# Kernel tuning notes

Hardware: AMD Instinct MI355X
Metric: run time of the kernel (lower is better)

The kernel has to match this reference:

```python
import jax, jax.numpy as jnp
import numpy as np

D_MODEL = 1024
NUM_HEADS = 16
HEAD_DIM = D_MODEL // NUM_HEADS
BATCH, SEQ = 2, 2048


def setup_inputs() -> dict:
    key = jax.random.key(0)
    k1, k2, k3, k4, k5 = jax.random.split(key, 5)
    x = jax.random.normal(k1, (BATCH, SEQ, D_MODEL), dtype=jnp.float32)
    mask = jnp.ones((BATCH, SEQ), dtype=jnp.int32)
    s = 1.0 / np.sqrt(D_MODEL)
    W_qkv = jax.random.uniform(k2, (D_MODEL, 3 * D_MODEL), jnp.float32, -s, s)
    b_qkv = jax.random.uniform(k3, (3 * D_MODEL,), jnp.float32, -s, s)
    W_proj = jax.random.uniform(k4, (D_MODEL, D_MODEL), jnp.float32, -s, s)
    b_proj = jax.random.uniform(k5, (D_MODEL,), jnp.float32, -s, s)
    return {"x": x, "mask": mask, "W_qkv": W_qkv, "b_qkv": b_qkv,
            "W_proj": W_proj, "b_proj": b_proj}


def reference(x, mask, W_qkv, b_qkv, W_proj, b_proj):
    B, S, _ = x.shape
    qkv = x @ W_qkv + b_qkv                                  # [B,S,3D]
    q, k, v = jnp.split(qkv, 3, axis=-1)
    def heads(t):  # [B,S,D] -> [B,H,S,hd]
        return t.reshape(B, S, NUM_HEADS, HEAD_DIM).transpose(0, 2, 1, 3)
    q, k, v = heads(q), heads(k), heads(v)
    scores = jnp.einsum('bhqd,bhkd->bhqk', q, k) / np.sqrt(HEAD_DIM)
    # mask: [B,S] key-padding -> [B,1,1,S], positions where mask==0 get -inf
    scores = jnp.where(mask[:, None, None, :] == 0, -jnp.inf, scores)
    attn = jax.nn.softmax(scores, axis=-1)
    ctx = jnp.einsum('bhqk,bhkd->bhqd', attn, v)             # [B,H,S,hd]
    ctx = ctx.transpose(0, 2, 1, 3).reshape(B, S, D_MODEL)
    return ctx @ W_proj + b_proj
```

## Files before the change

kernel.cpp:

```cpp
#include <hip/hip_runtime.h>


#define BATCH 2
#define SEQ 2048
#define DMODEL 1024
#define NHEADS 16
#define HDIM 64
#define BS (BATCH * SEQ)
#define N3 (3 * DMODEL)
#define QSCALE 0.18033688011112042f

typedef float f32x4 __attribute__((ext_vector_type(4)));
typedef float f32x16 __attribute__((ext_vector_type(16)));
typedef short bf16x8 __attribute__((ext_vector_type(8)));
typedef unsigned short u16;
typedef unsigned short u16x4 __attribute__((ext_vector_type(4)));

typedef const __attribute__((address_space(1))) unsigned int* gptr_t;
typedef __attribute__((address_space(3))) unsigned int* sptr_t;

__device__ __forceinline__ u16 f2bf(float f) {
  unsigned int u = __float_as_uint(f);
  return (u16)((u + 0x7fffu + ((u >> 16) & 1u)) >> 16);
}

__device__ __forceinline__ void gload_lds16(const void* g, void* l) {
  __builtin_amdgcn_global_load_lds((gptr_t)g, (sptr_t)l, 16, 0, 0);
}

__device__ __forceinline__ unsigned cvtpk(float lo, float hi) {
  unsigned r;
  asm("v_cvt_pk_bf16_f32 %0, %1, %2" : "=v"(r) : "v"(lo), "v"(hi));
  return r;
}

__device__ __forceinline__ void pl32swap(unsigned& d, unsigned& s) {
  asm volatile("v_permlane32_swap_b32 %0, %1" : "+v"(d), "+v"(s));
}

#define WAIT_VM4() asm volatile("s_waitcnt vmcnt(4)" ::: "memory")
#define WAIT_VM0() asm volatile("s_waitcnt vmcnt(0)" ::: "memory")

__global__ __launch_bounds__(256) void conv_x(const float* __restrict__ in,
                                              u16* __restrict__ out, int n4) {
  int i = blockIdx.x * 256 + threadIdx.x;
  if (i >= n4) return;
  float4 v = ((const float4*)in)[i];
  u16x4 o;
  o[0] = f2bf(v.x); o[1] = f2bf(v.y); o[2] = f2bf(v.z); o[3] = f2bf(v.w);
  ((u16x4*)out)[i] = o;
}

__global__ __launch_bounds__(256) void transp(const float* __restrict__ in,
                                              u16* __restrict__ out, int R, int C) {
  __shared__ float tile[64][65];
  int tx = threadIdx.x & 63, ty = threadIdx.x >> 6;
  int c0 = blockIdx.x * 64, r0 = blockIdx.y * 64;
#pragma unroll
  for (int j = ty; j < 64; j += 4)
    tile[j][tx] = in[(size_t)(r0 + j) * C + c0 + tx];
  __syncthreads();
#pragma unroll
  for (int j = ty; j < 64; j += 4)
    out[(size_t)(c0 + j) * R + r0 + tx] = f2bf(tile[tx][j]);
}

template <int MODE>
__global__ __launch_bounds__(256) void gemm_bt(
    const u16* __restrict__ A, const u16* __restrict__ Bt,
    const float* __restrict__ bias, float* __restrict__ outf,
    u16* __restrict__ qkb, u16* __restrict__ vtb, int M, int N, int K) {
  __shared__ __align__(16) u16 lds[3 * 2 * 4096];
  const int nwgx = gridDim.x;
  const int nwg = nwgx * gridDim.y;
  const int idx = blockIdx.y * nwgx + blockIdx.x;
  const int swz = (idx & 7) * (nwg >> 3) + (idx >> 3);
  const int m0 = (swz / nwgx) * 128, n0 = (swz % nwgx) * 128;

  const int tid = threadIdx.x;
  const int lane = tid & 63, w = tid >> 6;
  const int wr = w >> 1, wc = w & 1;
  const int lg = lane >> 4, lr = lane & 15;
  const int NK = K >> 5;

  f32x4 acc[4][4] = {};

  const int srow = tid >> 2;
  const int scb = (tid & 3) << 4;
  const char* Abase = (const char*)A + ((size_t)(m0 + srow) * K) * 2 + scb;
  const char* Bbase = (const char*)Bt + ((size_t)(n0 + srow) * K) * 2 + scb;
  const size_t half = (size_t)64 * K * 2;

  auto stage = [&](int buf, int kk) {
    char* dst = (char*)lds + buf * 16384;
    const char* a = Abase + kk * 64;
    gload_lds16(a, dst + tid * 16);
    gload_lds16(a + half, dst + 4096 + tid * 16);
    const char* b = Bbase + kk * 64;
    gload_lds16(b, dst + 8192 + tid * 16);
    gload_lds16(b + half, dst + 12288 + tid * 16);
  };

  stage(0, 0);
  stage(1, 1);
  int bi = 0;
  for (int kk = 0; kk < NK; ++kk) {
    if (kk < NK - 1) WAIT_VM4(); else WAIT_VM0();
    __builtin_amdgcn_s_barrier();
    if (kk + 2 < NK) stage(bi == 0 ? 2 : bi - 1, kk + 2);
    const u16* lA = lds + bi * 8192;
    const u16* lB = lA + 4096;
    bf16x8 af[4], bfr[4];
#pragma unroll
    for (int i = 0; i < 4; ++i)
      af[i] = *(const bf16x8*)(lA + (wr * 64 + i * 16 + lr) * 32 + lg * 8);
#pragma unroll
    for (int j = 0; j < 4; ++j)
      bfr[j] = *(const bf16x8*)(lB + (wc * 64 + j * 16 + lr) * 32 + lg * 8);
#pragma unroll
    for (int i = 0; i < 4; ++i)
#pragma unroll
      for (int j = 0; j < 4; ++j)
        acc[i][j] = __builtin_amdgcn_mfma_f32_16x16x32_bf16(af[i], bfr[j],
                                                            acc[i][j], 0, 0, 0);
    bi = (bi == 2) ? 0 : bi + 1;
  }

#pragma unroll
  for (int i = 0; i < 4; ++i) {
    const int rowb = m0 + wr * 64 + i * 16 + lg * 4;
#pragma unroll
    for (int j = 0; j < 4; ++j) {
      const int col = n0 + wc * 64 + j * 16 + lr;
      const float bv = bias[col];
      if (MODE == 0) {
        if (col < 2 * DMODEL) {
          const float qs = (col < DMODEL) ? QSCALE : 1.0f;
#pragma unroll
          for (int r = 0; r < 4; ++r)
            qkb[(size_t)(rowb + r) * (2 * DMODEL) + col] =
                f2bf((acc[i][j][r] + bv) * qs);
        } else {
          const int hd = col - 2 * DMODEL;
          const int b = rowb >> 11, s0 = rowb & (SEQ - 1);
          u16x4 pk;
#pragma unroll
          for (int r = 0; r < 4; ++r) pk[r] = f2bf(acc[i][j][r] + bv);
          *(u16x4*)(vtb +
                    ((size_t)((b * NHEADS + (hd >> 6)) * HDIM + (hd & 63))) * SEQ +
                    s0) = pk;
        }
      } else {
#pragma unroll
        for (int r = 0; r < 4; ++r)
          outf[(size_t)(rowb + r) * N + col] = acc[i][j][r] + bv;
      }
    }
  }
}

__global__ __launch_bounds__(256) void attn(const u16* __restrict__ qkb,
                                            const u16* __restrict__ vtb,
                                            const int* __restrict__ mask,
                                            u16* __restrict__ ctxb) {
  __shared__ __align__(16) u16 KV[3][2][64 * 64];
  __shared__ int anyz_l;

  const int idx = (blockIdx.z * gridDim.y + blockIdx.y) * gridDim.x + blockIdx.x;
  const int swz = (idx & 7) * 64 + (idx >> 3);
  const int q0 = (swz & 15) * 128;
  const int h = (swz >> 4) & 15;
  const int b = swz >> 8;

  const int tid = threadIdx.x;
  const int lane = tid & 63, w = tid >> 6;
  const int qi = lane & 31;
  const int hi = lane >> 5;
  const int q = q0 + w * 32 + qi;

  if (tid == 0) anyz_l = 0;
  __syncthreads();
  {
    const int4* mrow = (const int4*)(mask + b * SEQ);
    int z = 0;
#pragma unroll
    for (int i = 0; i < 2; ++i) {
      int4 m = mrow[tid + i * 256];
      z |= (m.x == 0) | (m.y == 0) | (m.z == 0) | (m.w == 0);
    }
    if (z) anyz_l = 1;
  }
  __syncthreads();
  const bool anyz = anyz_l != 0;

  bf16x8 qreg[4];
  {
    const u16* Qrow = qkb + (size_t)(b * SEQ + q) * (2 * DMODEL) + h * HDIM;
#pragma unroll
    for (int kc = 0; kc < 4; ++kc)
      qreg[kc] = *(const bf16x8*)(Qrow + kc * 16 + hi * 8);
  }

  float m_run = -3.0e38f, l_run = 0.f;
  f32x16 ct0 = (f32x16)0.f, ct1 = (f32x16)0.f;

  const u16* Kg = qkb + (size_t)(b * SEQ) * (2 * DMODEL) + DMODEL + h * HDIM;
  const u16* Vg = vtb + (size_t)((b * NHEADS + h) * HDIM) * SEQ;
  const int srow = tid >> 3;
  const int scol = ((tid & 7) ^ (srow & 7)) << 4;

  auto stage = [&](int buf, int t) {
    const int k0 = t * 64;
    const char* ks = (const char*)(Kg + (size_t)(k0 + srow) * (2 * DMODEL)) + scol;
    gload_lds16(ks, (char*)KV[buf][0] + tid * 16);
    gload_lds16(ks + (size_t)32 * (2 * DMODEL) * 2,
                (char*)KV[buf][0] + 4096 + tid * 16);
    const char* vs = (const char*)(Vg + (size_t)srow * SEQ + k0) + scol;
    gload_lds16(vs, (char*)KV[buf][1] + tid * 16);
    gload_lds16(vs + (size_t)32 * SEQ * 2, (char*)KV[buf][1] + 4096 + tid * 16);
  };

  auto compute = [&](int buf, int t, bool use_mask) {
    f32x16 s0 = (f32x16)0.f, s1 = (f32x16)0.f;
    const char* Kb = (const char*)KV[buf][0];
    __builtin_amdgcn_s_setprio(1);
#pragma unroll
    for (int kc = 0; kc < 4; ++kc) {
      const int sl = (((kc << 1) | hi) ^ (lane & 7)) << 4;
      bf16x8 kf0 = *(const bf16x8*)(Kb + qi * 128 + sl);
      bf16x8 kf1 = *(const bf16x8*)(Kb + (32 + qi) * 128 + sl);
      s0 = __builtin_amdgcn_mfma_f32_32x32x16_bf16(kf0, qreg[kc], s0, 0, 0, 0);
      s1 = __builtin_amdgcn_mfma_f32_32x32x16_bf16(kf1, qreg[kc], s1, 0, 0, 0);
    }
    __builtin_amdgcn_s_setprio(0);

    if (use_mask) {
      const int base = b * SEQ + t * 64;
#pragma unroll
      for (int r = 0; r < 16; ++r) {
        const int key = (r & 3) + 8 * (r >> 2) + 4 * hi;
        if (mask[base + key] == 0) s0[r] = -3.0e38f;
        if (mask[base + 32 + key] == 0) s1[r] = -3.0e38f;
      }
    }

    float pm = s0[0];
#pragma unroll
    for (int r = 1; r < 16; ++r) pm = fmaxf(pm, s0[r]);
#pragma unroll
    for (int r = 0; r < 16; ++r) pm = fmaxf(pm, s1[r]);
    pm = fmaxf(pm, __shfl_xor(pm, 32));
    if (__any(pm > m_run + 8.f)) {
      const float mn = fmaxf(m_run, pm);
      const float corr = __builtin_amdgcn_exp2f(m_run - mn);
      m_run = mn;
      l_run *= corr;
#pragma unroll
      for (int r = 0; r < 16; ++r) { ct0[r] *= corr; ct1[r] *= corr; }
    }
    float ls = 0.f;
#pragma unroll
    for (int r = 0; r < 16; ++r) {
      s0[r] = __builtin_amdgcn_exp2f(s0[r] - m_run); ls += s0[r];
    }
#pragma unroll
    for (int r = 0; r < 16; ++r) {
      s1[r] = __builtin_amdgcn_exp2f(s1[r] - m_run); ls += s1[r];
    }
    l_run += ls + __shfl_xor(ls, 32);

    unsigned pk[16];
#pragma unroll
    for (int rp = 0; rp < 8; ++rp) {
      pk[rp] = cvtpk(s0[2 * rp], s0[2 * rp + 1]);
      pk[8 + rp] = cvtpk(s1[2 * rp], s1[2 * rp + 1]);
    }

    const char* Vb = (const char*)KV[buf][1];
    __builtin_amdgcn_s_setprio(1);
#pragma unroll
    for (int ks = 0; ks < 4; ++ks) {
      const int mb = (ks >> 1) * 8 + (ks & 1) * 4;
      unsigned b0 = pk[mb + 0], b2 = pk[mb + 2];
      unsigned b1 = pk[mb + 1], b3 = pk[mb + 3];
      pl32swap(b0, b2);
      pl32swap(b1, b3);
      union { unsigned u[4]; bf16x8 v; } bu;
      bu.u[0] = b0; bu.u[1] = b1; bu.u[2] = b2; bu.u[3] = b3;
      const int sl = (((ks << 1) | hi) ^ (lane & 7)) << 4;
      bf16x8 vf0 = *(const bf16x8*)(Vb + qi * 128 + sl);
      bf16x8 vf1 = *(const bf16x8*)(Vb + (32 + qi) * 128 + sl);
      ct0 = __builtin_amdgcn_mfma_f32_32x32x16_bf16(vf0, bu.v, ct0, 0, 0, 0);
      ct1 = __builtin_amdgcn_mfma_f32_32x32x16_bf16(vf1, bu.v, ct1, 0, 0, 0);
    }
    __builtin_amdgcn_s_setprio(0);
  };

  const int NT = SEQ / 64;
  stage(0, 0);
  stage(1, 1);
  int bi = 0;
  if (!anyz) {
    for (int t = 0; t < NT; ++t) {
      if (t < NT - 1) WAIT_VM4(); else WAIT_VM0();
      __builtin_amdgcn_s_barrier();
      if (t + 2 < NT) stage(bi == 0 ? 2 : bi - 1, t + 2);
      compute(bi, t, false);
      bi = (bi == 2) ? 0 : bi + 1;
    }
  } else {
    for (int t = 0; t < NT; ++t) {
      __syncthreads();
      if (t + 2 < NT) stage(bi == 0 ? 2 : bi - 1, t + 2);
      __syncthreads();
      compute(bi, t, true);
      bi = (bi == 2) ? 0 : bi + 1;
    }
  }

  const float rl = __builtin_amdgcn_rcpf(l_run);
  u16* orow = ctxb + (size_t)(b * SEQ + q) * DMODEL + h * HDIM;
#pragma unroll
  for (int g = 0; g < 4; ++g) {
    {
      const int d0 = 8 * g + 4 * hi;
      uint2 st;
      st.x = cvtpk(ct0[4 * g] * rl, ct0[4 * g + 1] * rl);
      st.y = cvtpk(ct0[4 * g + 2] * rl, ct0[4 * g + 3] * rl);
      *(uint2*)(orow + d0) = st;
    }
    {
      const int d0 = 32 + 8 * g + 4 * hi;
      uint2 st;
      st.x = cvtpk(ct1[4 * g] * rl, ct1[4 * g + 1] * rl);
      st.y = cvtpk(ct1[4 * g + 2] * rl, ct1[4 * g + 3] * rl);
      *(uint2*)(orow + d0) = st;
    }
  }
}

extern "C" void kernel_launch(void* const* d_in, const int* in_sizes, int n_in,
                              void* d_out, int out_size, void* d_ws, size_t ws_size,
                              hipStream_t stream) {
  const float* x = (const float*)d_in[0];
  const int* mask = (const int*)d_in[1];
  const float* Wqkv = (const float*)d_in[2];
  const float* bqkv = (const float*)d_in[3];
  const float* Wproj = (const float*)d_in[4];
  const float* bproj = (const float*)d_in[5];
  float* out = (float*)d_out;

  char* ws = (char*)d_ws;
  u16* xb = (u16*)(ws);
  u16* wqkvt = (u16*)(ws + 8388608);
  u16* wprojt = (u16*)(ws + 14680064);
  u16* qkb = (u16*)(ws + 16777216);
  u16* vtb = (u16*)(ws + 33554432);
  u16* ctxb = (u16*)(ws + 41943040);

  conv_x<<<dim3((BS * DMODEL / 4 + 255) / 256), 256, 0, stream>>>(x, xb,
                                                                  BS * DMODEL / 4);
  transp<<<dim3(N3 / 64, DMODEL / 64), 256, 0, stream>>>(Wqkv, wqkvt, DMODEL, N3);
  transp<<<dim3(DMODEL / 64, DMODEL / 64), 256, 0, stream>>>(Wproj, wprojt, DMODEL,
                                                             DMODEL);
  gemm_bt<0><<<dim3(N3 / 128, BS / 128), 256, 0, stream>>>(
      xb, wqkvt, bqkv, nullptr, qkb, vtb, BS, N3, DMODEL);
  attn<<<dim3(SEQ / 128, NHEADS, BATCH), 256, 0, stream>>>(qkb, vtb, mask, ctxb);
  gemm_bt<1><<<dim3(DMODEL / 128, BS / 128), 256, 0, stream>>>(
      ctxb, wprojt, bproj, out, nullptr, nullptr, BS, DMODEL, DMODEL);
}
```

Before: 201.9 us.

## Software-pipeline attention: overlap next tile QK^T with previous tile PV

```diff
diff --git a/kernel.cpp b/kernel.cpp
--- a/kernel.cpp
+++ b/kernel.cpp
@@ -163,8 +163,8 @@
                                             const u16* __restrict__ vtb,
                                             const int* __restrict__ mask,
                                             u16* __restrict__ ctxb) {
-  __shared__ __align__(16) u16 KV[3][2][64 * 64];
-  __shared__ int anyz_l;
+  __shared__ __align__(16) u16 Kl[3][64 * 64];
+  __shared__ __align__(16) u16 Vl[4][64 * 64];
 
   const int idx = (blockIdx.z * gridDim.y + blockIdx.y) * gridDim.x + blockIdx.x;
   const int swz = (idx & 7) * 64 + (idx >> 3);
@@ -178,20 +178,17 @@
   const int hi = lane >> 5;
   const int q = q0 + w * 32 + qi;
 
-  if (tid == 0) anyz_l = 0;
-  __syncthreads();
+  bool anyz;
   {
     const int4* mrow = (const int4*)(mask + b * SEQ);
     int z = 0;
 #pragma unroll
-    for (int i = 0; i < 2; ++i) {
-      int4 m = mrow[tid + i * 256];
+    for (int p = 0; p < 8; ++p) {
+      int4 m = mrow[lane + p * 64];
       z |= (m.x == 0) | (m.y == 0) | (m.z == 0) | (m.w == 0);
     }
-    if (z) anyz_l = 1;
-  }
-  __syncthreads();
-  const bool anyz = anyz_l != 0;
+    anyz = __any(z);
+  }
 
   bf16x8 qreg[4];
   {
@@ -209,20 +206,20 @@
   const int srow = tid >> 3;
   const int scol = ((tid & 7) ^ (srow & 7)) << 4;
 
-  auto stage = [&](int buf, int t) {
+  auto stage = [&](int t) {
+    const int kb = t % 3, vb = t & 3;
     const int k0 = t * 64;
     const char* ks = (const char*)(Kg + (size_t)(k0 + srow) * (2 * DMODEL)) + scol;
-    gload_lds16(ks, (char*)KV[buf][0] + tid * 16);
+    gload_lds16(ks, (char*)Kl[kb] + tid * 16);
     gload_lds16(ks + (size_t)32 * (2 * DMODEL) * 2,
-                (char*)KV[buf][0] + 4096 + tid * 16);
+                (char*)Kl[kb] + 4096 + tid * 16);
     const char* vs = (const char*)(Vg + (size_t)srow * SEQ + k0) + scol;
-    gload_lds16(vs, (char*)KV[buf][1] + tid * 16);
-    gload_lds16(vs + (size_t)32 * SEQ * 2, (char*)KV[buf][1] + 4096 + tid * 16);
-  };
-
-  auto compute = [&](int buf, int t, bool use_mask) {
-    f32x16 s0 = (f32x16)0.f, s1 = (f32x16)0.f;
-    const char* Kb = (const char*)KV[buf][0];
+    gload_lds16(vs, (char*)Vl[vb] + tid * 16);
+    gload_lds16(vs + (size_t)32 * SEQ * 2, (char*)Vl[vb] + 4096 + tid * 16);
+  };
+
+  auto qkt = [&](int t, f32x16& s0, f32x16& s1) {
+    const char* Kb = (const char*)Kl[t % 3];
     __builtin_amdgcn_s_setprio(1);
 #pragma unroll
     for (int kc = 0; kc < 4; ++kc) {
@@ -233,50 +230,10 @@
       s1 = __builtin_amdgcn_mfma_f32_32x32x16_bf16(kf1, qreg[kc], s1, 0, 0, 0);
     }
     __builtin_amdgcn_s_setprio(0);
-
-    if (use_mask) {
-      const int base = b * SEQ + t * 64;
-#pragma unroll
-      for (int r = 0; r < 16; ++r) {
-        const int key = (r & 3) + 8 * (r >> 2) + 4 * hi;
-        if (mask[base + key] == 0) s0[r] = -3.0e38f;
-        if (mask[base + 32 + key] == 0) s1[r] = -3.0e38f;
-      }
-    }
-
-    float pm = s0[0];
-#pragma unroll
-    for (int r = 1; r < 16; ++r) pm = fmaxf(pm, s0[r]);
-#pragma unroll
-    for (int r = 0; r < 16; ++r) pm = fmaxf(pm, s1[r]);
-    pm = fmaxf(pm, __shfl_xor(pm, 32));
-    if (__any(pm > m_run + 8.f)) {
-      const float mn = fmaxf(m_run, pm);
-      const float corr = __builtin_amdgcn_exp2f(m_run - mn);
-      m_run = mn;
-      l_run *= corr;
-#pragma unroll
-      for (int r = 0; r < 16; ++r) { ct0[r] *= corr; ct1[r] *= corr; }
-    }
-    float ls = 0.f;
-#pragma unroll
-    for (int r = 0; r < 16; ++r) {
-      s0[r] = __builtin_amdgcn_exp2f(s0[r] - m_run); ls += s0[r];
-    }
-#pragma unroll
-    for (int r = 0; r < 16; ++r) {
-      s1[r] = __builtin_amdgcn_exp2f(s1[r] - m_run); ls += s1[r];
-    }
-    l_run += ls + __shfl_xor(ls, 32);
-
-    unsigned pk[16];
-#pragma unroll
-    for (int rp = 0; rp < 8; ++rp) {
-      pk[rp] = cvtpk(s0[2 * rp], s0[2 * rp + 1]);
-      pk[8 + rp] = cvtpk(s1[2 * rp], s1[2 * rp + 1]);
-    }
-
-    const char* Vb = (const char*)KV[buf][1];
+  };
+
+  auto pv = [&](int t, const unsigned pk[16]) {
+    const char* Vb = (const char*)Vl[t & 3];
     __builtin_amdgcn_s_setprio(1);
 #pragma unroll
     for (int ks = 0; ks < 4; ++ks) {
@@ -296,25 +253,80 @@
     __builtin_amdgcn_s_setprio(0);
   };
 
+  auto softmax = [&](f32x16& s0, f32x16& s1, int t, bool use_mask,
+                     unsigned pk[16]) {
+    if (use_mask) {
+      const int base = b * SEQ + t * 64;
+#pragma unroll
+      for (int r = 0; r < 16; ++r) {
+        const int key = (r & 3) + 8 * (r >> 2) + 4 * hi;
+        if (mask[base + key] == 0) s0[r] = -3.0e38f;
+        if (mask[base + 32 + key] == 0) s1[r] = -3.0e38f;
+      }
+    }
+    float pm = fmaxf(fmaxf(s0[0], s0[1]), s0[2]);
+#pragma unroll
+    for (int r = 3; r < 16; r += 2) pm = fmaxf(fmaxf(pm, s0[r]), s0[r + 1]);
+#pragma unroll
+    for (int r = 0; r < 16; r += 2) pm = fmaxf(fmaxf(pm, s1[r]), s1[r + 1]);
+    pm = fmaxf(pm, __shfl_xor(pm, 32));
+    if (__any(pm > m_run + 8.f)) {
+      const float mn = fmaxf(m_run, pm);
+      const float corr = __builtin_amdgcn_exp2f(m_run - mn);
+      m_run = mn;
+      l_run *= corr;
+#pragma unroll
+      for (int r = 0; r < 16; ++r) { ct0[r] *= corr; ct1[r] *= corr; }
+    }
+    float ls = 0.f;
+#pragma unroll
+    for (int r = 0; r < 16; ++r) {
+      s0[r] = __builtin_amdgcn_exp2f(s0[r] - m_run); ls += s0[r];
+    }
+#pragma unroll
+    for (int r = 0; r < 16; ++r) {
+      s1[r] = __builtin_amdgcn_exp2f(s1[r] - m_run); ls += s1[r];
+    }
+    l_run += ls + __shfl_xor(ls, 32);
+#pragma unroll
+    for (int rp = 0; rp < 8; ++rp) {
+      pk[rp] = cvtpk(s0[2 * rp], s0[2 * rp + 1]);
+      pk[8 + rp] = cvtpk(s1[2 * rp], s1[2 * rp + 1]);
+    }
+  };
+
   const int NT = SEQ / 64;
-  stage(0, 0);
-  stage(1, 1);
-  int bi = 0;
+  unsigned pkp[16];
+  stage(0);
+  stage(1);
   if (!anyz) {
-    for (int t = 0; t < NT; ++t) {
+    WAIT_VM4();
+    __builtin_amdgcn_s_barrier();
+    stage(2);
+    {
+      f32x16 s0 = (f32x16)0.f, s1 = (f32x16)0.f;
+      qkt(0, s0, s1);
+      softmax(s0, s1, 0, false, pkp);
+    }
+    for (int t = 1; t < NT; ++t) {
       if (t < NT - 1) WAIT_VM4(); else WAIT_VM0();
       __builtin_amdgcn_s_barrier();
-      if (t + 2 < NT) stage(bi == 0 ? 2 : bi - 1, t + 2);
-      compute(bi, t, false);
-      bi = (bi == 2) ? 0 : bi + 1;
-    }
+      if (t + 2 < NT) stage(t + 2);
+      f32x16 s0 = (f32x16)0.f, s1 = (f32x16)0.f;
+      qkt(t, s0, s1);
+      pv(t - 1, pkp);
+      softmax(s0, s1, t, false, pkp);
+    }
+    pv(NT - 1, pkp);
   } else {
     for (int t = 0; t < NT; ++t) {
       __syncthreads();
-      if (t + 2 < NT) stage(bi == 0 ? 2 : bi - 1, t + 2);
+      if (t + 2 < NT) stage(t + 2);
       __syncthreads();
-      compute(bi, t, true);
-      bi = (bi == 2) ? 0 : bi + 1;
+      f32x16 s0 = (f32x16)0.f, s1 = (f32x16)0.f;
+      qkt(t, s0, s1);
+      softmax(s0, s1, t, true, pkp);
+      pv(t, pkp);
     }
   }
 
```

Measured after the change: 199.2 us. No clear change (-1.3%).
